# Performance work log

Measured on AMD Instinct MI355X. Metric: run time of the kernel, lower is better.

The kernel has to match this reference:

```python
import jax, jax.numpy as jnp
import numpy as np

N, D, H, O, P = 50000, 256, 512, 64, 1024


def setup_inputs() -> dict:
    key = jax.random.key(0)
    ks = jax.random.split(key, 9)
    x = jax.random.normal(ks[0], (N, D), dtype=jnp.float32)
    W1 = jax.random.normal(ks[1], (H, D), dtype=jnp.float32) / np.sqrt(D)
    b1 = jax.random.normal(ks[2], (H,), dtype=jnp.float32) * 0.01
    W2 = jax.random.normal(ks[3], (O, H), dtype=jnp.float32) / np.sqrt(H)
    b2 = jax.random.normal(ks[4], (O,), dtype=jnp.float32) * 0.01
    ap = jax.random.randint(ks[5], (P,), 0, N, dtype=jnp.int32)
    p = jax.random.randint(ks[6], (P,), 0, N, dtype=jnp.int32)
    an = jax.random.randint(ks[7], (P,), 0, N, dtype=jnp.int32)
    n = jax.random.randint(ks[8], (P,), 0, N, dtype=jnp.int32)
    return {"x": x, "W1": W1, "b1": b1, "W2": W2, "b2": b2,
            "ap": ap, "p": p, "an": an, "n": n}


def reference(x, W1, b1, W2, b2, ap, p, an, n):
    """ContrastiveHessianCalculator.compute_hessian, loss_func='contrastive_full',
    wrt='weight', shape='diagonal', speed='half' (exact GGN diag), for the nnj net
    Linear(D,H) -> Tanh -> Linear(H,O).

    For a pair (x1,x2) the combined diag m0 - 2*m1 + m2 equals
    diag((J1-J2)^T (J1-J2)) where Ji = d f(xi)/d params. Closed form per layer:
      W1[i,j]: S11_i*x1_j^2 - 2*S12_i*x1_j*x2_j + S22_i*x2_j^2,
               Sab_i = tanh'(z1a)_i * tanh'(z1b)_i * sum_o W2[o,i]^2
      b1[i]:   S11_i - 2*S12_i + S22_i
      W2[i,j]: (h1_j - h2_j)^2  (independent of output row i)
      b2[i]:   0  (bias Jacobians of the two branches cancel)
    Per-layer diags are flattened [weight, bias] and concatenated (torch.cat(.., dim=1)),
    then summed over the pair batch; return sum(pos) - sum(neg).
    """
    c = jnp.sum(W2 * W2, axis=0)  # [H]

    def pair_hess_diag(ia, ib):
        xa = x[ia]            # [P, D]
        xb = x[ib]            # [P, D]
        ha = jnp.tanh(xa @ W1.T + b1)   # [P, H]
        hb = jnp.tanh(xb @ W1.T + b1)
        da = 1.0 - ha * ha              # tanh' at x_a, [P, H]
        db = 1.0 - hb * hb
        S11 = da * da * c               # [P, H]
        S12 = da * db * c
        S22 = db * db * c
        # W1 diag: [P, H, D]
        W1d = (S11[:, :, None] * (xa * xa)[:, None, :]
               - 2.0 * S12[:, :, None] * (xa * xb)[:, None, :]
               + S22[:, :, None] * (xb * xb)[:, None, :])
        b1d = S11 - 2.0 * S12 + S22      # [P, H]
        hd = (ha - hb) ** 2              # [P, H]
        W2d = jnp.broadcast_to(hd[:, None, :], (hd.shape[0], O, H))  # [P, O, H]
        b2d = jnp.zeros((hd.shape[0], O), dtype=hd.dtype)
        flat = jnp.concatenate([W1d.reshape(hd.shape[0], -1), b1d,
                                W2d.reshape(hd.shape[0], -1), b2d], axis=1)
        return jnp.sum(flat, axis=0)     # sum over pair batch -> [n_params]

    pos = pair_hess_diag(ap, p)
    neg = pair_hess_diag(an, n)
    return pos - neg
```

## Files before the change

### kernel.cpp

```cpp
#include <hip/hip_runtime.h>
#include <math.h>

#define DD_ 256
#define HH_ 512
#define OO_ 64

typedef __attribute__((ext_vector_type(8))) short bf16x8s;
typedef __attribute__((ext_vector_type(4))) float f32x4;

__device__ __forceinline__ unsigned short f2bf(float f) {
    unsigned u = __float_as_uint(f);
    u += 0x7FFF + ((u >> 16) & 1);
    return (unsigned short)(u >> 16);
}
__device__ __forceinline__ float bf2f(unsigned short h) {
    return __uint_as_float(((unsigned)h) << 16);
}
__device__ __forceinline__ int swz4(int r, int g) {
    return g ^ (r & 3) ^ ((r >> 2) & 3);
}

__global__ __launch_bounds__(256) void k_gemm1(
    const float* __restrict__ x, const float* __restrict__ W1, const float* __restrict__ b1,
    const int* __restrict__ i0p, const int* __restrict__ i1p,
    const int* __restrict__ i2p, const int* __restrict__ i3p,
    float* __restrict__ h) {
    __shared__ short Ah[64 * 32], Al[64 * 32], Bh[64 * 32], Bl[64 * 32];
    __shared__ int sidx[64];
    const int t = threadIdx.x;
    const int n0 = blockIdx.x * 64;
    const int rbase = blockIdx.y * 64;
    const int set = rbase >> 10;
    const int* I = (set == 0) ? i0p : (set == 1) ? i1p : (set == 2) ? i2p : i3p;
    if (t < 64) sidx[t] = I[(rbase & 1023) + t];
    __syncthreads();
    const int row = t >> 2, q = t & 3;
    const int l = t & 63, w = t >> 6;
    const int wm = w >> 1, wn = w & 1;
    const int lm = l & 15, g = l >> 4;
    const int sw = swz4(row, q);
    f32x4 acc[2][2] = {};
    for (int k0 = 0; k0 < DD_; k0 += 32) {
        {
            const float* src = x + (size_t)sidx[row] * DD_ + k0 + q * 8;
            float4 v0 = *(const float4*)src;
            float4 v1 = *(const float4*)(src + 4);
            float f[8] = {v0.x, v0.y, v0.z, v0.w, v1.x, v1.y, v1.z, v1.w};
            bf16x8s hi, lo;
            #pragma unroll
            for (int j = 0; j < 8; ++j) {
                unsigned short hh = f2bf(f[j]);
                hi[j] = (short)hh;
                lo[j] = (short)f2bf(f[j] - bf2f(hh));
            }
            *(bf16x8s*)(&Ah[(row * 4 + sw) * 8]) = hi;
            *(bf16x8s*)(&Al[(row * 4 + sw) * 8]) = lo;
        }
        {
            const float* src = W1 + (size_t)(n0 + row) * DD_ + k0 + q * 8;
            float4 v0 = *(const float4*)src;
            float4 v1 = *(const float4*)(src + 4);
            float f[8] = {v0.x, v0.y, v0.z, v0.w, v1.x, v1.y, v1.z, v1.w};
            bf16x8s hi, lo;
            #pragma unroll
            for (int j = 0; j < 8; ++j) {
                unsigned short hh = f2bf(f[j]);
                hi[j] = (short)hh;
                lo[j] = (short)f2bf(f[j] - bf2f(hh));
            }
            *(bf16x8s*)(&Bh[(row * 4 + sw) * 8]) = hi;
            *(bf16x8s*)(&Bl[(row * 4 + sw) * 8]) = lo;
        }
        __syncthreads();
        bf16x8s ah[2], al[2], bh[2], bl[2];
        #pragma unroll
        for (int mi = 0; mi < 2; ++mi) {
            int r = wm * 32 + mi * 16 + lm;
            ah[mi] = *(const bf16x8s*)(&Ah[(r * 4 + swz4(r, g)) * 8]);
            al[mi] = *(const bf16x8s*)(&Al[(r * 4 + swz4(r, g)) * 8]);
        }
        #pragma unroll
        for (int nj = 0; nj < 2; ++nj) {
            int r = wn * 32 + nj * 16 + lm;
            bh[nj] = *(const bf16x8s*)(&Bh[(r * 4 + swz4(r, g)) * 8]);
            bl[nj] = *(const bf16x8s*)(&Bl[(r * 4 + swz4(r, g)) * 8]);
        }
        #pragma unroll
        for (int mi = 0; mi < 2; ++mi)
            #pragma unroll
            for (int nj = 0; nj < 2; ++nj) {
                acc[mi][nj] = __builtin_amdgcn_mfma_f32_16x16x32_bf16(ah[mi], bh[nj], acc[mi][nj], 0, 0, 0);
                acc[mi][nj] = __builtin_amdgcn_mfma_f32_16x16x32_bf16(ah[mi], bl[nj], acc[mi][nj], 0, 0, 0);
                acc[mi][nj] = __builtin_amdgcn_mfma_f32_16x16x32_bf16(al[mi], bh[nj], acc[mi][nj], 0, 0, 0);
            }
        __syncthreads();
    }
    #pragma unroll
    for (int mi = 0; mi < 2; ++mi)
        #pragma unroll
        for (int nj = 0; nj < 2; ++nj) {
            int j = n0 + wn * 32 + nj * 16 + lm;
            float bv = b1[j];
            #pragma unroll
            for (int qq = 0; qq < 4; ++qq) {
                int r = rbase + wm * 32 + mi * 16 + g * 4 + qq;
                h[(size_t)r * HH_ + j] = tanhf(acc[mi][nj][qq] + bv);
            }
        }
}

__global__ __launch_bounds__(256) void k_build(
    const float* __restrict__ h, const float* __restrict__ x,
    const float* __restrict__ W2,
    const int* __restrict__ ap, const int* __restrict__ pI,
    const int* __restrict__ an, const int* __restrict__ nI,
    short* __restrict__ Mt, short* __restrict__ Xt,
    float* __restrict__ pb1, float* __restrict__ phd) {
    const int t = threadIdx.x;
    const int bb = blockIdx.x;
    if (bb < 256) {
        const int iblk = bb >> 5, pblk = bb & 31;
        const int i = iblk * 64 + (t >> 2), pq = t & 3;
        const int p0 = pblk * 64;
        const int s = p0 >> 10;
        const float sgn = s ? -1.f : 1.f;
        float ci = 0.f;
        #pragma unroll
        for (int o = 0; o < OO_; ++o) { float wv = W2[o * HH_ + i]; ci += wv * wv; }
        const int pb = (p0 & 1023) + pq * 16;
        const float* hA = h + (size_t)(s * 2048 + pb) * HH_ + i;
        const float* hB = hA + (size_t)1024 * HH_;
        short m[3][16];
        float b1p = 0.f, hdp = 0.f;
        #pragma unroll
        for (int pp = 0; pp < 16; ++pp) {
            float ha = hA[(size_t)pp * HH_];
            float hb = hB[(size_t)pp * HH_];
            float da = 1.f - ha * ha, db = 1.f - hb * hb;
            float s11 = sgn * (da * da * ci);
            float s12 = sgn * (-2.f * da * db * ci);
            float s22 = sgn * (db * db * ci);
            m[0][pp] = (short)f2bf(s11);
            m[1][pp] = (short)f2bf(s12);
            m[2][pp] = (short)f2bf(s22);
            b1p += s11 + s12 + s22;
            float d = ha - hb;
            hdp += sgn * d * d;
        }
        size_t base = (size_t)i * 6144 + p0 + pq * 16;
        #pragma unroll
        for (int term = 0; term < 3; ++term) {
            bf16x8s v0, v1;
            #pragma unroll
            for (int j2 = 0; j2 < 8; ++j2) { v0[j2] = m[term][j2]; v1[j2] = m[term][j2 + 8]; }
            *(bf16x8s*)(&Mt[base + (size_t)term * 2048]) = v0;
            *(bf16x8s*)(&Mt[base + (size_t)term * 2048 + 8]) = v1;
        }
        b1p += __shfl_xor(b1p, 1); b1p += __shfl_xor(b1p, 2);
        hdp += __shfl_xor(hdp, 1); hdp += __shfl_xor(hdp, 2);
        if (pq == 0) { pb1[pblk * HH_ + i] = b1p; phd[pblk * HH_ + i] = hdp; }
    } else {
        __shared__ int sia[64], sib[64];
        const int b2 = bb - 256;
        const int jblk = b2 >> 5, pblk = b2 & 31;
        const int j = jblk * 64 + (t >> 2), pq = t & 3;
        const int p0 = pblk * 64;
        const int s = p0 >> 10;
        const int* IA = s ? an : ap;
        const int* IB = s ? nI : pI;
        if (t < 64) sia[t] = IA[(p0 & 1023) + t];
        else if (t < 128) sib[t - 64] = IB[(p0 & 1023) + (t - 64)];
        __syncthreads();
        short xv[3][16];
        #pragma unroll
        for (int pp = 0; pp < 16; ++pp) {
            int pl = pq * 16 + pp;
            float xa = x[(size_t)sia[pl] * DD_ + j];
            float xb = x[(size_t)sib[pl] * DD_ + j];
            xv[0][pp] = (short)f2bf(xa * xa);
            xv[1][pp] = (short)f2bf(xa * xb);
            xv[2][pp] = (short)f2bf(xb * xb);
        }
        size_t base = (size_t)j * 6144 + p0 + pq * 16;
        #pragma unroll
        for (int term = 0; term < 3; ++term) {
            bf16x8s v0, v1;
            #pragma unroll
            for (int j2 = 0; j2 < 8; ++j2) { v0[j2] = xv[term][j2]; v1[j2] = xv[term][j2 + 8]; }
            *(bf16x8s*)(&Xt[base + (size_t)term * 2048]) = v0;
            *(bf16x8s*)(&Xt[base + (size_t)term * 2048 + 8]) = v1;
        }
    }
}

__global__ __launch_bounds__(256) void k_gemm2(
    const short* __restrict__ Mt, const short* __restrict__ Xt,
    float* __restrict__ part) {
    __shared__ short As[64 * 32], Bs[64 * 32];
    const int t = threadIdx.x;
    const int j0 = blockIdx.x * 64;
    const int i0 = blockIdx.y * 64;
    const int kb = blockIdx.z;
    const int row = t >> 2, q = t & 3;
    const int l = t & 63, w = t >> 6;
    const int wm = w >> 1, wn = w & 1;
    const int lm = l & 15, g = l >> 4;
    const int sw = swz4(row, q);
    f32x4 acc[2][2] = {};
    for (int ks = 0; ks < 12; ++ks) {
        const int k0 = kb * 384 + ks * 32;
        *(bf16x8s*)(&As[(row * 4 + sw) * 8]) =
            *(const bf16x8s*)(&Mt[(size_t)(i0 + row) * 6144 + k0 + q * 8]);
        *(bf16x8s*)(&Bs[(row * 4 + sw) * 8]) =
            *(const bf16x8s*)(&Xt[(size_t)(j0 + row) * 6144 + k0 + q * 8]);
        __syncthreads();
        bf16x8s a[2], b[2];
        #pragma unroll
        for (int mi = 0; mi < 2; ++mi) {
            int r = wm * 32 + mi * 16 + lm;
            a[mi] = *(const bf16x8s*)(&As[(r * 4 + swz4(r, g)) * 8]);
        }
        #pragma unroll
        for (int nj = 0; nj < 2; ++nj) {
            int r = wn * 32 + nj * 16 + lm;
            b[nj] = *(const bf16x8s*)(&Bs[(r * 4 + swz4(r, g)) * 8]);
        }
        #pragma unroll
        for (int mi = 0; mi < 2; ++mi)
            #pragma unroll
            for (int nj = 0; nj < 2; ++nj)
                acc[mi][nj] = __builtin_amdgcn_mfma_f32_16x16x32_bf16(a[mi], b[nj], acc[mi][nj], 0, 0, 0);
        __syncthreads();
    }
    #pragma unroll
    for (int mi = 0; mi < 2; ++mi)
        #pragma unroll
        for (int nj = 0; nj < 2; ++nj) {
            int j = j0 + wn * 32 + nj * 16 + lm;
            #pragma unroll
            for (int qq = 0; qq < 4; ++qq) {
                int i = i0 + wm * 32 + mi * 16 + g * 4 + qq;
                part[((size_t)kb * HH_ + i) * DD_ + j] = acc[mi][nj][qq];
            }
        }
}

__global__ void k_tail(const float* __restrict__ part, const float* __restrict__ pb1,
                       const float* __restrict__ phd, float* __restrict__ out) {
    int gid = blockIdx.x * 256 + threadIdx.x;
    const int HD = HH_ * DD_;
    if (gid < HD) {
        float sv = 0.f;
        #pragma unroll
        for (int kb = 0; kb < 16; ++kb) sv += part[(size_t)kb * HD + gid];
        out[gid] = sv;
    } else if (gid < HD + HH_) {
        int i = gid - HD;
        float sv = 0.f;
        #pragma unroll
        for (int kb = 0; kb < 32; ++kb) sv += pb1[kb * HH_ + i];
        out[gid] = sv;
    } else if (gid < HD + HH_ + OO_ * HH_) {
        int i = (gid - HD - HH_) & (HH_ - 1);
        float sv = 0.f;
        #pragma unroll
        for (int kb = 0; kb < 32; ++kb) sv += phd[kb * HH_ + i];
        out[gid] = sv;
    } else if (gid < HD + HH_ + OO_ * HH_ + OO_) {
        out[gid] = 0.f;
    }
}

extern "C" void kernel_launch(void* const* d_in, const int* in_sizes, int n_in,
                              void* d_out, int out_size, void* d_ws, size_t ws_size,
                              hipStream_t stream) {
    const float* x  = (const float*)d_in[0];
    const float* W1 = (const float*)d_in[1];
    const float* b1 = (const float*)d_in[2];
    const float* W2 = (const float*)d_in[3];
    const int* ap = (const int*)d_in[5];
    const int* pI = (const int*)d_in[6];
    const int* an = (const int*)d_in[7];
    const int* nI = (const int*)d_in[8];
    float* out = (float*)d_out;
    float* ws = (float*)d_ws;

    float* h    = ws;
    float* part = ws + 2097152;
    short* Mt   = (short*)(ws + 4194304);
    short* Xt   = (short*)(ws + 5767168);
    float* pb1  = ws + 6553600;
    float* phd  = ws + 6569984;

    k_gemm1<<<dim3(8, 64), dim3(256), 0, stream>>>(x, W1, b1, ap, pI, an, nI, h);
    k_build<<<dim3(384), dim3(256), 0, stream>>>(h, x, W2, ap, pI, an, nI, Mt, Xt, pb1, phd);
    k_gemm2<<<dim3(4, 8, 16), dim3(256), 0, stream>>>(Mt, Xt, part);
    k_tail<<<dim3(643), dim3(256), 0, stream>>>(part, pb1, phd, out);
}
```

Before: 36.36 us.

## Precompute bf16 hi/lo splits of gathered x and W1 in a prep kernel

A new prep kernel gathers the indexed x rows and W1 once and splits them into bf16 hi/lo halves. It also computes the W2 column norms and builds the Xt product terms, all before GEMM1. Before this, every gemm1 tile block redid the split inside its K loop, and each build block recomputed the 64-term norm. GEMM1 now just loads pre-split bf16, and the build stage drops to an M-only kernel. The cost is an extra launch and extra workspace traffic for the split copies.

```diff
diff --git a/kernel.cpp b/kernel.cpp
--- a/kernel.cpp
+++ b/kernel.cpp
@@ -20,148 +20,40 @@
     return g ^ (r & 3) ^ ((r >> 2) & 3);
 }
 
-__global__ __launch_bounds__(256) void k_gemm1(
-    const float* __restrict__ x, const float* __restrict__ W1, const float* __restrict__ b1,
-    const int* __restrict__ i0p, const int* __restrict__ i1p,
-    const int* __restrict__ i2p, const int* __restrict__ i3p,
-    float* __restrict__ h) {
-    __shared__ short Ah[64 * 32], Al[64 * 32], Bh[64 * 32], Bl[64 * 32];
-    __shared__ int sidx[64];
+__global__ __launch_bounds__(256) void k_prep(
+    const float* __restrict__ x, const float* __restrict__ W1, const float* __restrict__ W2,
+    const int* __restrict__ ap, const int* __restrict__ pI,
+    const int* __restrict__ an, const int* __restrict__ nI,
+    short* __restrict__ xhi, short* __restrict__ xlo,
+    short* __restrict__ w1hi, short* __restrict__ w1lo,
+    float* __restrict__ c, short* __restrict__ Xt) {
     const int t = threadIdx.x;
-    const int n0 = blockIdx.x * 64;
-    const int rbase = blockIdx.y * 64;
-    const int set = rbase >> 10;
-    const int* I = (set == 0) ? i0p : (set == 1) ? i1p : (set == 2) ? i2p : i3p;
-    if (t < 64) sidx[t] = I[(rbase & 1023) + t];
-    __syncthreads();
-    const int row = t >> 2, q = t & 3;
-    const int l = t & 63, w = t >> 6;
-    const int wm = w >> 1, wn = w & 1;
-    const int lm = l & 15, g = l >> 4;
-    const int sw = swz4(row, q);
-    f32x4 acc[2][2] = {};
-    for (int k0 = 0; k0 < DD_; k0 += 32) {
-        {
-            const float* src = x + (size_t)sidx[row] * DD_ + k0 + q * 8;
-            float4 v0 = *(const float4*)src;
-            float4 v1 = *(const float4*)(src + 4);
+    const int bb = blockIdx.x;
+    if (bb < 64) {
+        const int r = bb * 64 + (t >> 2), q = t & 3;
+        const int set = r >> 10;
+        const int* I = (set == 0) ? ap : (set == 1) ? pI : (set == 2) ? an : nI;
+        const int idx = I[r & 1023];
+        const float* src = x + (size_t)idx * DD_ + q * 64;
+        const size_t dst = (size_t)r * DD_ + q * 64;
+        #pragma unroll
+        for (int jj = 0; jj < 8; ++jj) {
+            float4 v0 = *(const float4*)(src + jj * 8);
+            float4 v1 = *(const float4*)(src + jj * 8 + 4);
             float f[8] = {v0.x, v0.y, v0.z, v0.w, v1.x, v1.y, v1.z, v1.w};
             bf16x8s hi, lo;
             #pragma unroll
-            for (int j = 0; j < 8; ++j) {
-                unsigned short hh = f2bf(f[j]);
-                hi[j] = (short)hh;
-                lo[j] = (short)f2bf(f[j] - bf2f(hh));
-            }
-            *(bf16x8s*)(&Ah[(row * 4 + sw) * 8]) = hi;
-            *(bf16x8s*)(&Al[(row * 4 + sw) * 8]) = lo;
-        }
-        {
-            const float* src = W1 + (size_t)(n0 + row) * DD_ + k0 + q * 8;
-            float4 v0 = *(const float4*)src;
-            float4 v1 = *(const float4*)(src + 4);
-            float f[8] = {v0.x, v0.y, v0.z, v0.w, v1.x, v1.y, v1.z, v1.w};
-            bf16x8s hi, lo;
-            #pragma unroll
-            for (int j = 0; j < 8; ++j) {
-                unsigned short hh = f2bf(f[j]);
-                hi[j] = (short)hh;
-                lo[j] = (short)f2bf(f[j] - bf2f(hh));
-            }
-            *(bf16x8s*)(&Bh[(row * 4 + sw) * 8]) = hi;
-            *(bf16x8s*)(&Bl[(row * 4 + sw) * 8]) = lo;
-        }
-        __syncthreads();
-        bf16x8s ah[2], al[2], bh[2], bl[2];
-        #pragma unroll
-        for (int mi = 0; mi < 2; ++mi) {
-            int r = wm * 32 + mi * 16 + lm;
-            ah[mi] = *(const bf16x8s*)(&Ah[(r * 4 + swz4(r, g)) * 8]);
-            al[mi] = *(const bf16x8s*)(&Al[(r * 4 + swz4(r, g)) * 8]);
-        }
-        #pragma unroll
-        for (int nj = 0; nj < 2; ++nj) {
-            int r = wn * 32 + nj * 16 + lm;
-            bh[nj] = *(const bf16x8s*)(&Bh[(r * 4 + swz4(r, g)) * 8]);
-            bl[nj] = *(const bf16x8s*)(&Bl[(r * 4 + swz4(r, g)) * 8]);
-        }
-        #pragma unroll
-        for (int mi = 0; mi < 2; ++mi)
-            #pragma unroll
-            for (int nj = 0; nj < 2; ++nj) {
-                acc[mi][nj] = __builtin_amdgcn_mfma_f32_16x16x32_bf16(ah[mi], bh[nj], acc[mi][nj], 0, 0, 0);
-                acc[mi][nj] = __builtin_amdgcn_mfma_f32_16x16x32_bf16(ah[mi], bl[nj], acc[mi][nj], 0, 0, 0);
-                acc[mi][nj] = __builtin_amdgcn_mfma_f32_16x16x32_bf16(al[mi], bh[nj], acc[mi][nj], 0, 0, 0);
-            }
-        __syncthreads();
-    }
-    #pragma unroll
-    for (int mi = 0; mi < 2; ++mi)
-        #pragma unroll
-        for (int nj = 0; nj < 2; ++nj) {
-            int j = n0 + wn * 32 + nj * 16 + lm;
-            float bv = b1[j];
-            #pragma unroll
-            for (int qq = 0; qq < 4; ++qq) {
-                int r = rbase + wm * 32 + mi * 16 + g * 4 + qq;
-                h[(size_t)r * HH_ + j] = tanhf(acc[mi][nj][qq] + bv);
-            }
-        }
-}
-
-__global__ __launch_bounds__(256) void k_build(
-    const float* __restrict__ h, const float* __restrict__ x,
-    const float* __restrict__ W2,
-    const int* __restrict__ ap, const int* __restrict__ pI,
-    const int* __restrict__ an, const int* __restrict__ nI,
-    short* __restrict__ Mt, short* __restrict__ Xt,
-    float* __restrict__ pb1, float* __restrict__ phd) {
-    const int t = threadIdx.x;
-    const int bb = blockIdx.x;
-    if (bb < 256) {
-        const int iblk = bb >> 5, pblk = bb & 31;
-        const int i = iblk * 64 + (t >> 2), pq = t & 3;
-        const int p0 = pblk * 64;
-        const int s = p0 >> 10;
-        const float sgn = s ? -1.f : 1.f;
-        float ci = 0.f;
-        #pragma unroll
-        for (int o = 0; o < OO_; ++o) { float wv = W2[o * HH_ + i]; ci += wv * wv; }
-        const int pb = (p0 & 1023) + pq * 16;
-        const float* hA = h + (size_t)(s * 2048 + pb) * HH_ + i;
-        const float* hB = hA + (size_t)1024 * HH_;
-        short m[3][16];
-        float b1p = 0.f, hdp = 0.f;
-        #pragma unroll
-        for (int pp = 0; pp < 16; ++pp) {
-            float ha = hA[(size_t)pp * HH_];
-            float hb = hB[(size_t)pp * HH_];
-            float da = 1.f - ha * ha, db = 1.f - hb * hb;
-            float s11 = sgn * (da * da * ci);
-            float s12 = sgn * (-2.f * da * db * ci);
-            float s22 = sgn * (db * db * ci);
-            m[0][pp] = (short)f2bf(s11);
-            m[1][pp] = (short)f2bf(s12);
-            m[2][pp] = (short)f2bf(s22);
-            b1p += s11 + s12 + s22;
-            float d = ha - hb;
-            hdp += sgn * d * d;
-        }
-        size_t base = (size_t)i * 6144 + p0 + pq * 16;
-        #pragma unroll
-        for (int term = 0; term < 3; ++term) {
-            bf16x8s v0, v1;
-            #pragma unroll
-            for (int j2 = 0; j2 < 8; ++j2) { v0[j2] = m[term][j2]; v1[j2] = m[term][j2 + 8]; }
-            *(bf16x8s*)(&Mt[base + (size_t)term * 2048]) = v0;
-            *(bf16x8s*)(&Mt[base + (size_t)term * 2048 + 8]) = v1;
-        }
-        b1p += __shfl_xor(b1p, 1); b1p += __shfl_xor(b1p, 2);
-        hdp += __shfl_xor(hdp, 1); hdp += __shfl_xor(hdp, 2);
-        if (pq == 0) { pb1[pblk * HH_ + i] = b1p; phd[pblk * HH_ + i] = hdp; }
-    } else {
+            for (int e = 0; e < 8; ++e) {
+                unsigned short hh = f2bf(f[e]);
+                hi[e] = (short)hh;
+                lo[e] = (short)f2bf(f[e] - bf2f(hh));
+            }
+            *(bf16x8s*)(&xhi[dst + jj * 8]) = hi;
+            *(bf16x8s*)(&xlo[dst + jj * 8]) = lo;
+        }
+    } else if (bb < 192) {
         __shared__ int sia[64], sib[64];
-        const int b2 = bb - 256;
+        const int b2 = bb - 64;
         const int jblk = b2 >> 5, pblk = b2 & 31;
         const int j = jblk * 64 + (t >> 2), pq = t & 3;
         const int p0 = pblk * 64;
@@ -186,11 +78,141 @@
         for (int term = 0; term < 3; ++term) {
             bf16x8s v0, v1;
             #pragma unroll
-            for (int j2 = 0; j2 < 8; ++j2) { v0[j2] = xv[term][j2]; v1[j2] = xv[term][j2 + 8]; }
+            for (int e = 0; e < 8; ++e) { v0[e] = xv[term][e]; v1[e] = xv[term][e + 8]; }
             *(bf16x8s*)(&Xt[base + (size_t)term * 2048]) = v0;
             *(bf16x8s*)(&Xt[base + (size_t)term * 2048 + 8]) = v1;
         }
-    }
+    } else if (bb < 208) {
+        const int b3 = bb - 192;
+        const int r = b3 * 32 + (t >> 3), q = t & 7;
+        const float* src = W1 + (size_t)r * DD_ + q * 32;
+        const size_t dst = (size_t)r * DD_ + q * 32;
+        #pragma unroll
+        for (int jj = 0; jj < 4; ++jj) {
+            float4 v0 = *(const float4*)(src + jj * 8);
+            float4 v1 = *(const float4*)(src + jj * 8 + 4);
+            float f[8] = {v0.x, v0.y, v0.z, v0.w, v1.x, v1.y, v1.z, v1.w};
+            bf16x8s hi, lo;
+            #pragma unroll
+            for (int e = 0; e < 8; ++e) {
+                unsigned short hh = f2bf(f[e]);
+                hi[e] = (short)hh;
+                lo[e] = (short)f2bf(f[e] - bf2f(hh));
+            }
+            *(bf16x8s*)(&w1hi[dst + jj * 8]) = hi;
+            *(bf16x8s*)(&w1lo[dst + jj * 8]) = lo;
+        }
+    } else {
+        const int i = (bb - 208) * 256 + t;
+        float s = 0.f;
+        #pragma unroll
+        for (int o = 0; o < OO_; ++o) { float w = W2[o * HH_ + i]; s += w * w; }
+        c[i] = s;
+    }
+}
+
+__global__ __launch_bounds__(256) void k_gemm1(
+    const short* __restrict__ xhi, const short* __restrict__ xlo,
+    const short* __restrict__ w1hi, const short* __restrict__ w1lo,
+    const float* __restrict__ b1, float* __restrict__ h) {
+    __shared__ short Ah[64 * 32], Al[64 * 32], Bh[64 * 32], Bl[64 * 32];
+    const int t = threadIdx.x;
+    const int n0 = blockIdx.x * 64;
+    const int rbase = blockIdx.y * 64;
+    const int row = t >> 2, q = t & 3;
+    const int l = t & 63, w = t >> 6;
+    const int wm = w >> 1, wn = w & 1;
+    const int lm = l & 15, g = l >> 4;
+    const int sw = swz4(row, q);
+    f32x4 acc[2][2] = {};
+    for (int k0 = 0; k0 < DD_; k0 += 32) {
+        const size_t asrc = (size_t)(rbase + row) * DD_ + k0 + q * 8;
+        const size_t bsrc = (size_t)(n0 + row) * DD_ + k0 + q * 8;
+        *(bf16x8s*)(&Ah[(row * 4 + sw) * 8]) = *(const bf16x8s*)(&xhi[asrc]);
+        *(bf16x8s*)(&Al[(row * 4 + sw) * 8]) = *(const bf16x8s*)(&xlo[asrc]);
+        *(bf16x8s*)(&Bh[(row * 4 + sw) * 8]) = *(const bf16x8s*)(&w1hi[bsrc]);
+        *(bf16x8s*)(&Bl[(row * 4 + sw) * 8]) = *(const bf16x8s*)(&w1lo[bsrc]);
+        __syncthreads();
+        bf16x8s ah[2], al[2], bh[2], bl[2];
+        #pragma unroll
+        for (int mi = 0; mi < 2; ++mi) {
+            int r = wm * 32 + mi * 16 + lm;
+            ah[mi] = *(const bf16x8s*)(&Ah[(r * 4 + swz4(r, g)) * 8]);
+            al[mi] = *(const bf16x8s*)(&Al[(r * 4 + swz4(r, g)) * 8]);
+        }
+        #pragma unroll
+        for (int nj = 0; nj < 2; ++nj) {
+            int r = wn * 32 + nj * 16 + lm;
+            bh[nj] = *(const bf16x8s*)(&Bh[(r * 4 + swz4(r, g)) * 8]);
+            bl[nj] = *(const bf16x8s*)(&Bl[(r * 4 + swz4(r, g)) * 8]);
+        }
+        #pragma unroll
+        for (int mi = 0; mi < 2; ++mi)
+            #pragma unroll
+            for (int nj = 0; nj < 2; ++nj) {
+                acc[mi][nj] = __builtin_amdgcn_mfma_f32_16x16x32_bf16(ah[mi], bh[nj], acc[mi][nj], 0, 0, 0);
+                acc[mi][nj] = __builtin_amdgcn_mfma_f32_16x16x32_bf16(ah[mi], bl[nj], acc[mi][nj], 0, 0, 0);
+                acc[mi][nj] = __builtin_amdgcn_mfma_f32_16x16x32_bf16(al[mi], bh[nj], acc[mi][nj], 0, 0, 0);
+            }
+        __syncthreads();
+    }
+    #pragma unroll
+    for (int mi = 0; mi < 2; ++mi)
+        #pragma unroll
+        for (int nj = 0; nj < 2; ++nj) {
+            int j = n0 + wn * 32 + nj * 16 + lm;
+            float bv = b1[j];
+            #pragma unroll
+            for (int qq = 0; qq < 4; ++qq) {
+                int r = rbase + wm * 32 + mi * 16 + g * 4 + qq;
+                h[(size_t)r * HH_ + j] = tanhf(acc[mi][nj][qq] + bv);
+            }
+        }
+}
+
+__global__ __launch_bounds__(256) void k_buildM(
+    const float* __restrict__ h, const float* __restrict__ c,
+    short* __restrict__ Mt, float* __restrict__ pb1, float* __restrict__ phd) {
+    const int t = threadIdx.x;
+    const int bb = blockIdx.x;
+    const int iblk = bb >> 5, pblk = bb & 31;
+    const int i = iblk * 64 + (t >> 2), pq = t & 3;
+    const int p0 = pblk * 64;
+    const int s = p0 >> 10;
+    const float sgn = s ? -1.f : 1.f;
+    const float ci = c[i];
+    const int pb = (p0 & 1023) + pq * 16;
+    const float* hA = h + (size_t)(s * 2048 + pb) * HH_ + i;
+    const float* hB = hA + (size_t)1024 * HH_;
+    short m[3][16];
+    float b1p = 0.f, hdp = 0.f;
+    #pragma unroll
+    for (int pp = 0; pp < 16; ++pp) {
+        float ha = hA[(size_t)pp * HH_];
+        float hb = hB[(size_t)pp * HH_];
+        float da = 1.f - ha * ha, db = 1.f - hb * hb;
+        float s11 = sgn * (da * da * ci);
+        float s12 = sgn * (-2.f * da * db * ci);
+        float s22 = sgn * (db * db * ci);
+        m[0][pp] = (short)f2bf(s11);
+        m[1][pp] = (short)f2bf(s12);
+        m[2][pp] = (short)f2bf(s22);
+        b1p += s11 + s12 + s22;
+        float d = ha - hb;
+        hdp += sgn * d * d;
+    }
+    size_t base = (size_t)i * 6144 + p0 + pq * 16;
+    #pragma unroll
+    for (int term = 0; term < 3; ++term) {
+        bf16x8s v0, v1;
+        #pragma unroll
+        for (int e = 0; e < 8; ++e) { v0[e] = m[term][e]; v1[e] = m[term][e + 8]; }
+        *(bf16x8s*)(&Mt[base + (size_t)term * 2048]) = v0;
+        *(bf16x8s*)(&Mt[base + (size_t)term * 2048 + 8]) = v1;
+    }
+    b1p += __shfl_xor(b1p, 1); b1p += __shfl_xor(b1p, 2);
+    hdp += __shfl_xor(hdp, 1); hdp += __shfl_xor(hdp, 2);
+    if (pq == 0) { pb1[pblk * HH_ + i] = b1p; phd[pblk * HH_ + i] = hdp; }
 }
 
 __global__ __launch_bounds__(256) void k_gemm2(
@@ -291,9 +313,16 @@
     short* Xt   = (short*)(ws + 5767168);
     float* pb1  = ws + 6553600;
     float* phd  = ws + 6569984;
-
-    k_gemm1<<<dim3(8, 64), dim3(256), 0, stream>>>(x, W1, b1, ap, pI, an, nI, h);
-    k_build<<<dim3(384), dim3(256), 0, stream>>>(h, x, W2, ap, pI, an, nI, Mt, Xt, pb1, phd);
+    short* xhi  = (short*)(ws + 6586368);
+    short* xlo  = (short*)(ws + 7110656);
+    short* w1hi = (short*)(ws + 7634944);
+    short* w1lo = (short*)(ws + 7700480);
+    float* c    = ws + 7766016;
+
+    k_prep<<<dim3(210), dim3(256), 0, stream>>>(x, W1, W2, ap, pI, an, nI,
+                                                xhi, xlo, w1hi, w1lo, c, Xt);
+    k_gemm1<<<dim3(8, 64), dim3(256), 0, stream>>>(xhi, xlo, w1hi, w1lo, b1, h);
+    k_buildM<<<dim3(256), dim3(256), 0, stream>>>(h, c, Mt, pb1, phd);
     k_gemm2<<<dim3(4, 8, 16), dim3(256), 0, stream>>>(Mt, Xt, part);
     k_tail<<<dim3(643), dim3(256), 0, stream>>>(part, pb1, phd, out);
 }
```

Result: slower. 41.83 us (+15.0%).
